# Performance work log

Measured on AMD Instinct MI355X. Metric: run time of the kernel, lower is better.

## Reference

```python
import jax, jax.numpy as jnp
import numpy as np

DIM = 192
HEADS = 4
EPS = 1e-12  # F.normalize default eps


def setup_inputs() -> dict:
    key = jax.random.key(0)
    ks = jax.random.split(key, 5)
    b, c, h, w = 8, DIM, 128, 128
    x = jax.random.normal(ks[0], (b, c, h, w), dtype=jnp.float32)
    w_qkv = jax.random.normal(ks[1], (3 * DIM, DIM, 1, 1), dtype=jnp.float32) * (1.0 / np.sqrt(DIM))
    w_dw = jax.random.normal(ks[2], (3 * DIM, 1, 3, 3), dtype=jnp.float32) * (1.0 / 3.0)
    w_proj = jax.random.normal(ks[3], (DIM, DIM, 1, 1), dtype=jnp.float32) * (1.0 / np.sqrt(DIM))
    temperature = jnp.ones((HEADS, 1, 1), dtype=jnp.float32)
    return {"x": x, "w_qkv": w_qkv, "w_dw": w_dw, "w_proj": w_proj, "temperature": temperature}


def _conv1x1(x, w):
    # x: [b,c,h,w], w: [o,c,1,1] -> [b,o,h,w]
    return jnp.einsum('bchw,oc->bohw', x, w[:, :, 0, 0])


def _dwconv3x3(x, w):
    # depthwise 3x3, padding=1; x: [b,C,h,w], w: [C,1,3,3]
    C = x.shape[1]
    return jax.lax.conv_general_dilated(
        x, w, window_strides=(1, 1), padding=((1, 1), (1, 1)),
        dimension_numbers=('NCHW', 'OIHW', 'NCHW'), feature_group_count=C)


def _l2norm(x):
    n = jnp.linalg.norm(x, axis=-1, keepdims=True)
    return x / jnp.maximum(n, EPS)


def reference(x, w_qkv, w_dw, w_proj, temperature):
    b, c, h, w = x.shape
    head = HEADS
    ch = c // head  # channels per head
    qkv = _dwconv3x3(_conv1x1(x, w_qkv), w_dw)  # [b, 3c, h, w]
    q, k, v = jnp.split(qkv, 3, axis=1)  # each [b, c, h, w]

    def to_heads(t):
        # b (head ch) h w -> b head h (ch w)
        t = t.reshape(b, head, ch, h, w)
        return t.transpose(0, 1, 3, 2, 4).reshape(b, head, h, ch * w)

    q1 = _l2norm(to_heads(q))
    k1 = _l2norm(to_heads(k))
    v1 = to_heads(v)
    # attn over height dim: [b, head, h, h]
    attn = jax.nn.softmax(jnp.einsum('bhif,bhjf->bhij', q1, k1) * temperature[None], axis=-1)
    out = jnp.einsum('bhij,bhjf->bhif', attn, v1)  # [b, head, h, ch*w]
    # b head h (ch w) -> b (head ch) h w
    out = out.reshape(b, head, h, ch, w).transpose(0, 1, 3, 2, 4).reshape(b, c, h, w)
    return _conv1x1(out, w_proj)
```

## Files before the change

### kernel.cpp

```cpp
#include <hip/hip_runtime.h>
#include <hip/hip_bf16.h>

#define BB 8
#define CC 192
#define C3 576
#define NH 4
#define CH 48
#define HH 128
#define WW 128
#define HW 16384
#define FF 6144

typedef short s16x8 __attribute__((ext_vector_type(8)));
typedef float f32x4 __attribute__((ext_vector_type(4)));

constexpr size_t SPM = 32ull * 128 * 128;

constexpr size_t OFF_XT  = 0;
constexpr size_t SZ_XT   = (size_t)BB * HW * CC * 2;
constexpr size_t OFF_WQ  = OFF_XT + SZ_XT;
constexpr size_t SZ_WQ   = (size_t)C3 * CC * 2;
constexpr size_t OFF_WP  = OFF_WQ + SZ_WQ;
constexpr size_t SZ_WP   = (size_t)CC * CC * 2;
constexpr size_t OFF_RAW = OFF_WP + SZ_WP;
constexpr size_t SZ_RAW  = (size_t)BB * C3 * HW * 2;
constexpr size_t OFF_DW  = OFF_RAW + SZ_RAW;
constexpr size_t OFF_SP  = OFF_DW + SZ_RAW;
constexpr size_t OFF_ATB = OFF_SP + 8 * SPM * 4;
constexpr size_t OFF_RQ  = OFF_ATB + 32ull * 128 * 128 * 2;
constexpr size_t OFF_RK  = OFF_RQ + 32 * 128 * 4;
constexpr size_t OFF_PS  = OFF_SP;

__device__ __forceinline__ short bf16bits(float v) {
  __hip_bfloat16 t = __float2bfloat16(v);
  return *reinterpret_cast<short*>(&t);
}
__device__ __forceinline__ float b2f(short u) {
  union { unsigned int i; float f; } x;
  x.i = ((unsigned int)(unsigned short)u) << 16;
  return x.f;
}

__device__ __forceinline__ void gload16(const void* g, void* l) {
  __builtin_amdgcn_global_load_lds((const __attribute__((address_space(1))) unsigned int*)g,
                                   (__attribute__((address_space(3))) unsigned int*)l, 16, 0, 0);
}

__device__ __forceinline__ void vmdrain() { asm volatile("s_waitcnt vmcnt(0)" ::: "memory"); }

__global__ __launch_bounds__(256) void k_cvt_t(const float* __restrict__ in,
                                               __hip_bfloat16* __restrict__ outT) {
  const int p0 = blockIdx.x * 64;
  const int c0 = blockIdx.y * 32;
  const int b = blockIdx.z;
  __shared__ float t[32][65];
  const float* ib = in + (size_t)b * CC * HW;
  const int tid = threadIdx.x;
  {
    const int c = tid >> 3, pl = (tid & 7) * 8;
    const float* s = ib + (size_t)(c0 + c) * HW + p0 + pl;
#pragma unroll
    for (int j = 0; j < 8; ++j) t[c][pl + j] = s[j];
  }
  __syncthreads();
  {
    const int pl = tid >> 2, cl = (tid & 3) * 8;
    __hip_bfloat16* d = outT + (size_t)b * HW * CC + (size_t)(p0 + pl) * CC + c0 + cl;
#pragma unroll
    for (int j = 0; j < 8; ++j) d[j] = __float2bfloat16(t[cl + j][pl]);
  }
}

__global__ __launch_bounds__(256) void k_cvt_w2(const float* __restrict__ in1, int n1,
                                                const float* __restrict__ in2, int n2,
                                                __hip_bfloat16* __restrict__ out) {
  const int i = blockIdx.x * 256 + threadIdx.x;
  if (i < n1) out[i] = __float2bfloat16(in1[i]);
  else if (i < n1 + n2) out[i] = __float2bfloat16(in2[i - n1]);
}

__global__ __launch_bounds__(256) void k_gemm(const __hip_bfloat16* __restrict__ xT,
                                              const __hip_bfloat16* __restrict__ Wb,
                                              __hip_bfloat16* __restrict__ out) {
  const int pBase = blockIdx.x * 128;
  const int mBase = blockIdx.y * 96;
  const int b = blockIdx.z;
  __shared__ char smem[28672];
  const int tid = threadIdx.x;
  const int wave = tid >> 6, lane = tid & 63;
  const int wm = wave >> 1, wn = wave & 1;
  const __hip_bfloat16* xb = xT + (size_t)b * HW * CC;
  f32x4 acc[3][4] = {};

  auto stage = [&](int k0, int buf) {
    char* Alc = smem + buf * 6144;
    char* Blc = smem + 12288 + buf * 8192;
    {
      const int ci = tid;
      const int row = ci & 15, kg = (ci >> 4) & 3, mf = ci >> 6;
      gload16(Wb + (size_t)(mBase + mf * 16 + row) * CC + k0 + kg * 8,
              Alc + wave * 1024);
    }
    if (tid < 128) {
      const int ci = 256 + tid;
      const int row = ci & 15, kg = (ci >> 4) & 3, mf = ci >> 6;
      gload16(Wb + (size_t)(mBase + mf * 16 + row) * CC + k0 + kg * 8,
              Alc + 4096 + wave * 1024);
    }
#pragma unroll
    for (int is = 0; is < 2; ++is) {
      const int ci = is * 256 + tid;
      const int col = ci & 15, kg = (ci >> 4) & 3, nf = ci >> 6;
      gload16(xb + (size_t)(pBase + nf * 16 + col) * CC + k0 + kg * 8,
              Blc + is * 4096 + wave * 1024);
    }
  };

  stage(0, 0);
  vmdrain();
  __syncthreads();
  for (int kc = 0; kc < 6; ++kc) {
    const int cur = kc & 1;
    if (kc < 5) stage((kc + 1) * 32, cur ^ 1);
    char* Alc = smem + cur * 6144;
    char* Blc = smem + 12288 + cur * 8192;
    s16x8 a[3], bf[4];
#pragma unroll
    for (int i = 0; i < 3; ++i) a[i] = *(const s16x8*)(Alc + ((wm * 3 + i) << 10) + (lane << 4));
#pragma unroll
    for (int j = 0; j < 4; ++j) bf[j] = *(const s16x8*)(Blc + ((wn * 4 + j) << 10) + (lane << 4));
#pragma unroll
    for (int i = 0; i < 3; ++i)
#pragma unroll
      for (int j = 0; j < 4; ++j)
        acc[i][j] = __builtin_amdgcn_mfma_f32_16x16x32_bf16(a[i], bf[j], acc[i][j], 0, 0, 0);
    vmdrain();
    __syncthreads();
  }
  short* E = (short*)smem;
  const int r0 = (lane >> 4) * 4, cl = lane & 15;
#pragma unroll
  for (int i = 0; i < 3; ++i) {
    const int lr = wm * 48 + i * 16 + r0;
#pragma unroll
    for (int j = 0; j < 4; ++j) {
      const int col = (wn * 4 + j) * 16 + cl;
#pragma unroll
      for (int r = 0; r < 4; ++r) E[(lr + r) * 136 + col] = bf16bits(acc[i][j][r]);
    }
  }
  __syncthreads();
  __hip_bfloat16* ob = out + (size_t)b * C3 * HW + pBase;
#pragma unroll
  for (int it = 0; it < 6; ++it) {
    const int vi = it * 256 + tid;
    const int row = vi >> 4, c8 = (vi & 15) * 8;
    const s16x8 v = *(const s16x8*)(E + row * 136 + c8);
    *(s16x8*)(ob + (size_t)(mBase + row) * HW + c8) = v;
  }
}

__global__ __launch_bounds__(256) void k_dwconv(const __hip_bfloat16* __restrict__ in,
                                                const float* __restrict__ wdw,
                                                __hip_bfloat16* __restrict__ out,
                                                __hip_bfloat16* __restrict__ vt,
                                                float* __restrict__ psum) {
  const int h0 = blockIdx.x * 32;
  const int c = blockIdx.y;
  const int b = blockIdx.z;
  __shared__ __hip_bfloat16 IN[34][152];
  __shared__ char TR[8192];
  const int tid = threadIdx.x;
  const __hip_bfloat16* src = in + ((size_t)b * C3 + c) * HW;
  if (tid < 68) {
    const int r = tid >> 1, col = (tid & 1) ? 136 : 0;
    *(s16x8*)(&IN[r][col]) = (s16x8){};
  }
#pragma unroll
  for (int it = 0; it < 3; ++it) {
    const int vi = it * 256 + tid;
    if (vi < 544) {
      const int r = vi >> 4, w8 = vi & 15;
      const int hg = h0 - 1 + r;
      s16x8 v = {};
      if (hg >= 0 && hg < HH) v = *(const s16x8*)(src + (size_t)hg * WW + w8 * 8);
      *(s16x8*)(&IN[r][8 + w8 * 8]) = v;
    }
  }
  const float* wp = wdw + c * 9;
  float wgt[9];
#pragma unroll
  for (int q = 0; q < 9; ++q) wgt[q] = wp[q];
  __syncthreads();

  const int hl = tid >> 3, w0 = (tid & 7) * 16;
  float res[16] = {};
#pragma unroll
  for (int dh = 0; dh < 3; ++dh) {
    const __hip_bfloat16* rp = &IN[hl + dh][0];
    const s16x8 v0 = *(const s16x8*)(rp + w0);
    const s16x8 v1 = *(const s16x8*)(rp + w0 + 8);
    const s16x8 v2 = *(const s16x8*)(rp + w0 + 16);
    const s16x8 v3 = *(const s16x8*)(rp + w0 + 24);
    float rv[18];
    rv[0] = b2f(v0[7]);
#pragma unroll
    for (int e = 0; e < 8; ++e) rv[1 + e] = b2f(v1[e]);
#pragma unroll
    for (int e = 0; e < 8; ++e) rv[9 + e] = b2f(v2[e]);
    rv[17] = b2f(v3[0]);
    const float wa = wgt[dh * 3], wb = wgt[dh * 3 + 1], wc = wgt[dh * 3 + 2];
#pragma unroll
    for (int ww = 0; ww < 16; ++ww)
      res[ww] += rv[ww] * wa + rv[ww + 1] * wb + rv[ww + 2] * wc;
  }
  if (c < 2 * CC) {
    short pk[16];
#pragma unroll
    for (int ww = 0; ww < 16; ++ww) pk[ww] = bf16bits(res[ww]);
    __hip_bfloat16* dst = out + ((size_t)b * C3 + c) * HW + (size_t)(h0 + hl) * WW + w0;
    *(s16x8*)dst = *(const s16x8*)pk;
    *(s16x8*)(dst + 8) = *(const s16x8*)(pk + 8);
    float ss = 0.f;
#pragma unroll
    for (int ww = 0; ww < 16; ++ww) ss += res[ww] * res[ww];
#pragma unroll
    for (int off = 4; off > 0; off >>= 1) ss += __shfl_down(ss, off);
    if ((tid & 7) == 0) psum[((size_t)b * HH + h0 + hl) * 384 + c] = ss;
  } else {
    const int rel = c - 2 * CC;
    const int hd = rel / CH, ch = rel - hd * CH;
#pragma unroll
    for (int ww = 0; ww < 16; ++ww) {
      const int w = w0 + ww;
      const int blk = ((w << 2) + (hl >> 3)) ^ ((w >> 3) & 3);
      *(short*)(TR + (blk << 4) + ((hl & 7) << 1)) = bf16bits(res[ww]);
    }
    __syncthreads();
    const int w = tid >> 1, hf = tid & 1;
    short ot[16];
#pragma unroll
    for (int j = 0; j < 2; ++j) {
      const int hh = hf * 16 + j * 8;
      const int blk = ((w << 2) + (hh >> 3)) ^ ((w >> 3) & 3);
      *(s16x8*)(ot + j * 8) = *(const s16x8*)(TR + (blk << 4));
    }
    __hip_bfloat16* vd = vt + ((size_t)(b * NH + hd) * FF + (size_t)ch * WW + w) * HH + h0 + hf * 16;
    *(s16x8*)vd = *(const s16x8*)ot;
    *(s16x8*)(vd + 8) = *(const s16x8*)(ot + 8);
  }
}

__global__ __launch_bounds__(64) void k_norms2(const float* __restrict__ psum,
                                               float* __restrict__ rq, float* __restrict__ rk) {
  const int i = blockIdx.x;
  const int hd = blockIdx.y;
  const int b = blockIdx.z & 7;
  const int which = blockIdx.z >> 3;
  const int lane = threadIdx.x;
  float s = 0.f;
  if (lane < 48) s = psum[((size_t)b * HH + i) * 384 + which * CC + hd * CH + lane];
#pragma unroll
  for (int off = 32; off > 0; off >>= 1) s += __shfl_down(s, off);
  if (lane == 0) {
    const float n = sqrtf(s);
    float* dst = which ? rk : rq;
    dst[(b * NH + hd) * HH + i] = 1.f / fmaxf(n, 1e-12f);
  }
}

__global__ __launch_bounds__(256) void k_qkm(const __hip_bfloat16* __restrict__ dw,
                                             float* __restrict__ sp) {
  const int ks = blockIdx.x;
  const int bh = blockIdx.y;
  const int b = bh >> 2, hd = bh & 3;
  const __hip_bfloat16* qb = dw + ((size_t)b * C3 + hd * CH) * HW;
  const __hip_bfloat16* kb = dw + ((size_t)b * C3 + CC + hd * CH) * HW;
  __shared__ __hip_bfloat16 Al[2][4096];
  __shared__ __hip_bfloat16 Bl[2][4096];
  const int tid = threadIdx.x, wave = tid >> 6, lane = tid & 63;
  const int wm = wave >> 1, wn = wave & 1;
  f32x4 acc[4][4] = {};

  auto stage = [&](int chunk, int buf) {
    const int ch = ks * 6 + (chunk >> 2);
    const int w0 = (chunk & 3) * 32;
    char* Alc = (char*)Al[buf];
    char* Blc = (char*)Bl[buf];
#pragma unroll
    for (int is = 0; is < 2; ++is) {
      const int ci = is * 256 + tid;
      const int row = ci & 15, kg = (ci >> 4) & 3, mf = ci >> 6;
      gload16(qb + (size_t)ch * HW + (mf * 16 + row) * WW + w0 + kg * 8,
              Alc + is * 4096 + wave * 1024);
    }
#pragma unroll
    for (int is = 0; is < 2; ++is) {
      const int ci = is * 256 + tid;
      const int col = ci & 15, kg = (ci >> 4) & 3, nf = ci >> 6;
      gload16(kb + (size_t)ch * HW + (nf * 16 + col) * WW + w0 + kg * 8,
              Blc + is * 4096 + wave * 1024);
    }
  };

  stage(0, 0);
  vmdrain();
  __syncthreads();
  for (int chunk = 0; chunk < 24; ++chunk) {
    const int cur = chunk & 1;
    if (chunk < 23) stage(chunk + 1, cur ^ 1);
    char* Alc = (char*)Al[cur];
    char* Blc = (char*)Bl[cur];
    s16x8 a[4], bf[4];
#pragma unroll
    for (int i = 0; i < 4; ++i) a[i] = *(const s16x8*)(Alc + ((wm * 4 + i) << 10) + (lane << 4));
#pragma unroll
    for (int j = 0; j < 4; ++j) bf[j] = *(const s16x8*)(Blc + ((wn * 4 + j) << 10) + (lane << 4));
#pragma unroll
    for (int i = 0; i < 4; ++i)
#pragma unroll
      for (int j = 0; j < 4; ++j)
        acc[i][j] = __builtin_amdgcn_mfma_f32_16x16x32_bf16(a[i], bf[j], acc[i][j], 0, 0, 0);
    vmdrain();
    __syncthreads();
  }
  float* o = sp + (size_t)ks * SPM + (size_t)bh * HH * HH;
  const int r0 = (lane >> 4) * 4, cl = lane & 15;
#pragma unroll
  for (int i = 0; i < 4; ++i)
#pragma unroll
    for (int j = 0; j < 4; ++j) {
      const int ii = wm * 64 + i * 16 + r0;
      const int jj = wn * 64 + j * 16 + cl;
#pragma unroll
      for (int r = 0; r < 4; ++r) o[(ii + r) * HH + jj] = acc[i][j][r];
    }
}

__global__ __launch_bounds__(256) void k_softmax(const float* __restrict__ sp,
                                                 const float* __restrict__ rq,
                                                 const float* __restrict__ rk,
                                                 const float* __restrict__ temp,
                                                 __hip_bfloat16* __restrict__ atb) {
  const int wave = threadIdx.x >> 6, lane = threadIdx.x & 63;
  const int i = blockIdx.x * 4 + wave;
  const int bh = blockIdx.y;
  const int hd = bh & 3;
  const size_t rowoff = ((size_t)bh * HH + i) * HH;
  float s0 = 0.f, s1 = 0.f;
#pragma unroll
  for (int ks = 0; ks < 8; ++ks) {
    s0 += sp[ks * SPM + rowoff + lane];
    s1 += sp[ks * SPM + rowoff + lane + 64];
  }
  const float scale = rq[bh * HH + i] * temp[hd];
  s0 *= scale * rk[bh * HH + lane];
  s1 *= scale * rk[bh * HH + lane + 64];
  float m = fmaxf(s0, s1);
#pragma unroll
  for (int off = 32; off > 0; off >>= 1) m = fmaxf(m, __shfl_xor(m, off));
  const float e0 = expf(s0 - m), e1 = expf(s1 - m);
  float ssum = e0 + e1;
#pragma unroll
  for (int off = 32; off > 0; off >>= 1) ssum += __shfl_xor(ssum, off);
  const float inv = 1.f / ssum;
  atb[rowoff + lane] = __float2bfloat16(e0 * inv);
  atb[rowoff + lane + 64] = __float2bfloat16(e1 * inv);
}

__global__ __launch_bounds__(256) void k_pvm(const __hip_bfloat16* __restrict__ atb,
                                             const __hip_bfloat16* __restrict__ vt,
                                             __hip_bfloat16* __restrict__ pvout) {
  const int fs = blockIdx.x;
  const int bh = blockIdx.y;
  const __hip_bfloat16* ab = atb + (size_t)bh * HH * HH;
  const __hip_bfloat16* vb = vt + ((size_t)bh * FF + fs * 128) * HH;
  __shared__ __hip_bfloat16 Al[2][4096];
  __shared__ __hip_bfloat16 Bl[2][4096];
  const int tid = threadIdx.x, wave = tid >> 6, lane = tid & 63;
  const int wm = wave >> 1, wn = wave & 1;
  f32x4 acc[4][4] = {};

  auto stage = [&](int kc, int buf) {
    const int kj0 = kc * 32;
    char* Alc = (char*)Al[buf];
    char* Blc = (char*)Bl[buf];
#pragma unroll
    for (int is = 0; is < 2; ++is) {
      const int ci = is * 256 + tid;
      const int row = ci & 15, kg = (ci >> 4) & 3, mf = ci >> 6;
      gload16(ab + (size_t)(mf * 16 + row) * HH + kj0 + kg * 8,
              Alc + is * 4096 + wave * 1024);
    }
#pragma unroll
    for (int is = 0; is < 2; ++is) {
      const int ci = is * 256 + tid;
      const int col = ci & 15, kg = (ci >> 4) & 3, nf = ci >> 6;
      gload16(vb + (size_t)(nf * 16 + col) * HH + kj0 + kg * 8,
              Blc + is * 4096 + wave * 1024);
    }
  };

  stage(0, 0);
  vmdrain();
  __syncthreads();
  for (int kc = 0; kc < 4; ++kc) {
    const int cur = kc & 1;
    if (kc < 3) stage(kc + 1, cur ^ 1);
    char* Alc = (char*)Al[cur];
    char* Blc = (char*)Bl[cur];
    s16x8 a[4], bf[4];
#pragma unroll
    for (int i = 0; i < 4; ++i) a[i] = *(const s16x8*)(Alc + ((wm * 4 + i) << 10) + (lane << 4));
#pragma unroll
    for (int j = 0; j < 4; ++j) bf[j] = *(const s16x8*)(Blc + ((wn * 4 + j) << 10) + (lane << 4));
#pragma unroll
    for (int i = 0; i < 4; ++i)
#pragma unroll
      for (int j = 0; j < 4; ++j)
        acc[i][j] = __builtin_amdgcn_mfma_f32_16x16x32_bf16(a[i], bf[j], acc[i][j], 0, 0, 0);
    vmdrain();
    __syncthreads();
  }
  __hip_bfloat16* ob = pvout + (size_t)bh * HH * FF;
  const int r0 = (lane >> 4) * 4, cl = lane & 15;
#pragma unroll
  for (int i = 0; i < 4; ++i)
#pragma unroll
    for (int j = 0; j < 4; ++j) {
      const int ii = wm * 64 + i * 16 + r0;
      const int f = fs * 128 + (wn * 4 + j) * 16 + cl;
#pragma unroll
      for (int r = 0; r < 4; ++r) ob[(size_t)(ii + r) * FF + f] = __float2bfloat16(acc[i][j][r]);
    }
}

__global__ __launch_bounds__(256) void k_proj(const __hip_bfloat16* __restrict__ pv,
                                              const __hip_bfloat16* __restrict__ Wp,
                                              float* __restrict__ out) {
  const int i = blockIdx.x;
  const int b = blockIdx.y;
  __shared__ __hip_bfloat16 Al[6144];
  __shared__ __hip_bfloat16 Braw[12288];
  __shared__ __hip_bfloat16 Bfrag[4096];
  char* Alc = (char*)Al;
  char* Brc = (char*)Braw;
  char* Bfc = (char*)Bfrag;
  const int tid = threadIdx.x, wave = tid >> 6, lane = tid & 63;
  const int wm = wave >> 1, wn = wave & 1;
  f32x4 acc[6][4] = {};
  for (int hf = 0; hf < 2; ++hf) {
    if (hf) __syncthreads();
#pragma unroll
    for (int it = 0; it < 6; ++it) {
      const int vi = it * 256 + tid;
      const int r = vi >> 4, w8 = vi & 15;
      const int hi = (r >= 48) ? 1 : 0;
      const int hd = hf * 2 + hi, ch = r - hi * 48;
      const s16x8 v = *(const s16x8*)(pv + ((size_t)(b * NH + hd) * HH + i) * FF + ch * 128 + w8 * 8);
      *(s16x8*)(Brc + r * 256 + ((w8 ^ (r & 15)) << 4)) = v;
    }
    __syncthreads();
    for (int kc = 0; kc < 3; ++kc) {
      const int c0 = hf * 96 + kc * 32;
#pragma unroll
      for (int is = 0; is < 3; ++is) {
        const int ci = is * 256 + tid;
        const int row = ci & 15, kg = (ci >> 4) & 3, mf = ci >> 6;
        gload16(Wp + (size_t)(mf * 16 + row) * CC + c0 + kg * 8,
                Alc + is * 4096 + wave * 1024);
      }
#pragma unroll
      for (int it = 0; it < 2; ++it) {
        const int vi = it * 256 + tid;
        const int col = vi & 15, kg = (vi >> 4) & 3, nf = vi >> 6;
        const int w = nf * 16 + col;
        short tmp[8];
#pragma unroll
        for (int e = 0; e < 8; ++e) {
          const int r = (kc * 4 + kg) * 8 + e;
          tmp[e] = *(const short*)(Brc + r * 256 + (((w >> 3) ^ (r & 15)) << 4) + (w & 7) * 2);
        }
        *(s16x8*)(Bfc + ((nf * 64 + kg * 16 + col) << 4)) = *(const s16x8*)tmp;
      }
      vmdrain();
      __syncthreads();
      s16x8 a[6], bf[4];
#pragma unroll
      for (int mi = 0; mi < 6; ++mi)
        a[mi] = *(const s16x8*)(Alc + ((wm * 6 + mi) << 10) + (lane << 4));
#pragma unroll
      for (int j = 0; j < 4; ++j)
        bf[j] = *(const s16x8*)(Bfc + (((wn * 4 + j) * 64 + lane) << 4));
#pragma unroll
      for (int mi = 0; mi < 6; ++mi)
#pragma unroll
        for (int j = 0; j < 4; ++j)
          acc[mi][j] = __builtin_amdgcn_mfma_f32_16x16x32_bf16(a[mi], bf[j], acc[mi][j], 0, 0, 0);
      __syncthreads();
    }
  }
  const int r0 = (lane >> 4) * 4, cl = lane & 15;
#pragma unroll
  for (int mi = 0; mi < 6; ++mi) {
    const int o = (wm * 6 + mi) * 16 + r0;
#pragma unroll
    for (int j = 0; j < 4; ++j) {
      const int w = (wn * 4 + j) * 16 + cl;
      float* dst = out + ((size_t)b * CC + o) * HW + i * 128 + w;
#pragma unroll
      for (int r = 0; r < 4; ++r) dst[(size_t)r * HW] = acc[mi][j][r];
    }
  }
}

extern "C" void kernel_launch(void* const* d_in, const int* in_sizes, int n_in,
                              void* d_out, int out_size, void* d_ws, size_t ws_size,
                              hipStream_t stream) {
  const float* x     = (const float*)d_in[0];
  const float* wqkv  = (const float*)d_in[1];
  const float* wdw   = (const float*)d_in[2];
  const float* wproj = (const float*)d_in[3];
  const float* temp  = (const float*)d_in[4];

  char* ws = (char*)d_ws;
  __hip_bfloat16* xTb    = (__hip_bfloat16*)(ws + OFF_XT);
  __hip_bfloat16* vt     = (__hip_bfloat16*)(ws + OFF_XT);
  __hip_bfloat16* Wq     = (__hip_bfloat16*)(ws + OFF_WQ);
  __hip_bfloat16* Wp     = (__hip_bfloat16*)(ws + OFF_WP);
  __hip_bfloat16* qkvraw = (__hip_bfloat16*)(ws + OFF_RAW);
  __hip_bfloat16* pvout  = (__hip_bfloat16*)(ws + OFF_RAW);
  __hip_bfloat16* qkvdw  = (__hip_bfloat16*)(ws + OFF_DW);
  float* sp    = (float*)(ws + OFF_SP);
  float* psum  = (float*)(ws + OFF_PS);
  __hip_bfloat16* atb = (__hip_bfloat16*)(ws + OFF_ATB);
  float* rq    = (float*)(ws + OFF_RQ);
  float* rk    = (float*)(ws + OFF_RK);

  k_cvt_w2<<<dim3((C3 * CC + CC * CC + 255) / 256), 256, 0, stream>>>(wqkv, C3 * CC, wproj, CC * CC, Wq);
  k_cvt_t<<<dim3(HW / 64, CC / 32, BB), 256, 0, stream>>>(x, xTb);
  k_gemm<<<dim3(HW / 128, C3 / 96, BB), 256, 0, stream>>>(xTb, Wq, qkvraw);
  k_dwconv<<<dim3(HH / 32, C3, BB), 256, 0, stream>>>(qkvraw, wdw, qkvdw, vt, psum);
  k_norms2<<<dim3(HH, NH, 2 * BB), 64, 0, stream>>>(psum, rq, rk);
  k_qkm<<<dim3(8, 32), 256, 0, stream>>>(qkvdw, sp);
  k_softmax<<<dim3(HH / 4, 32), 256, 0, stream>>>(sp, rq, rk, temp, atb);
  k_pvm<<<dim3(48, 32), 256, 0, stream>>>(atb, vt, pvout);
  k_proj<<<dim3(HH, BB), 256, 0, stream>>>(pvout, Wp, (float*)d_out);
}
```

Baseline: 271.7 us.

## Triple-buffer LDS staging with partial vmcnt waits in GEMM kernels

Switches the qkv GEMM, the QK^T kernel and the PV kernel from double-buffered to triple-buffered LDS staging. Loads now run two stages ahead, and the full vmcnt(0) drain plus __syncthreads is replaced by per-wave partial vmcnt waits and raw s_barrier calls. The aim is to keep global-to-LDS loads in flight while MFMAs run, hiding memory latency. In exchange the kernels use more shared memory, which may lower occupancy, and correctness depends on hand-counted vmcnt values per wave.

```diff
diff --git a/kernel.cpp b/kernel.cpp
--- a/kernel.cpp
+++ b/kernel.cpp
@@ -46,6 +46,7 @@
                                    (__attribute__((address_space(3))) unsigned int*)l, 16, 0, 0);
 }
 
+#define VMWAIT(N) asm volatile("s_waitcnt vmcnt(" #N ")" ::: "memory")
 __device__ __forceinline__ void vmdrain() { asm volatile("s_waitcnt vmcnt(0)" ::: "memory"); }
 
 __global__ __launch_bounds__(256) void k_cvt_t(const float* __restrict__ in,
@@ -85,7 +86,7 @@
   const int pBase = blockIdx.x * 128;
   const int mBase = blockIdx.y * 96;
   const int b = blockIdx.z;
-  __shared__ char smem[28672];
+  __shared__ char smem[43008];
   const int tid = threadIdx.x;
   const int wave = tid >> 6, lane = tid & 63;
   const int wm = wave >> 1, wn = wave & 1;
@@ -93,19 +94,17 @@
   f32x4 acc[3][4] = {};
 
   auto stage = [&](int k0, int buf) {
-    char* Alc = smem + buf * 6144;
-    char* Blc = smem + 12288 + buf * 8192;
+    char* Alc = smem + buf * 14336;
+    char* Blc = Alc + 6144;
     {
       const int ci = tid;
       const int row = ci & 15, kg = (ci >> 4) & 3, mf = ci >> 6;
-      gload16(Wb + (size_t)(mBase + mf * 16 + row) * CC + k0 + kg * 8,
-              Alc + wave * 1024);
+      gload16(Wb + (size_t)(mBase + mf * 16 + row) * CC + k0 + kg * 8, Alc + wave * 1024);
     }
     if (tid < 128) {
       const int ci = 256 + tid;
       const int row = ci & 15, kg = (ci >> 4) & 3, mf = ci >> 6;
-      gload16(Wb + (size_t)(mBase + mf * 16 + row) * CC + k0 + kg * 8,
-              Alc + 4096 + wave * 1024);
+      gload16(Wb + (size_t)(mBase + mf * 16 + row) * CC + k0 + kg * 8, Alc + 4096 + wave * 1024);
     }
 #pragma unroll
     for (int is = 0; is < 2; ++is) {
@@ -117,13 +116,17 @@
   };
 
   stage(0, 0);
-  vmdrain();
-  __syncthreads();
+  stage(32, 1);
+#pragma unroll
   for (int kc = 0; kc < 6; ++kc) {
-    const int cur = kc & 1;
-    if (kc < 5) stage((kc + 1) * 32, cur ^ 1);
-    char* Alc = smem + cur * 6144;
-    char* Blc = smem + 12288 + cur * 8192;
+    const int cur = kc % 3;
+    if (kc < 4) stage((kc + 2) * 32, (kc + 2) % 3);
+    if (kc < 4) { if (wave < 2) VMWAIT(8); else VMWAIT(6); }
+    else if (kc == 4) { if (wave < 2) VMWAIT(4); else VMWAIT(3); }
+    else VMWAIT(0);
+    __builtin_amdgcn_s_barrier();
+    char* Alc = smem + cur * 14336;
+    char* Blc = Alc + 6144;
     s16x8 a[3], bf[4];
 #pragma unroll
     for (int i = 0; i < 3; ++i) a[i] = *(const s16x8*)(Alc + ((wm * 3 + i) << 10) + (lane << 4));
@@ -134,8 +137,7 @@
 #pragma unroll
       for (int j = 0; j < 4; ++j)
         acc[i][j] = __builtin_amdgcn_mfma_f32_16x16x32_bf16(a[i], bf[j], acc[i][j], 0, 0, 0);
-    vmdrain();
-    __syncthreads();
+    __builtin_amdgcn_s_barrier();
   }
   short* E = (short*)smem;
   const int r0 = (lane >> 4) * 4, cl = lane & 15;
@@ -276,8 +278,7 @@
   const int b = bh >> 2, hd = bh & 3;
   const __hip_bfloat16* qb = dw + ((size_t)b * C3 + hd * CH) * HW;
   const __hip_bfloat16* kb = dw + ((size_t)b * C3 + CC + hd * CH) * HW;
-  __shared__ __hip_bfloat16 Al[2][4096];
-  __shared__ __hip_bfloat16 Bl[2][4096];
+  __shared__ char smem[49152];
   const int tid = threadIdx.x, wave = tid >> 6, lane = tid & 63;
   const int wm = wave >> 1, wn = wave & 1;
   f32x4 acc[4][4] = {};
@@ -285,8 +286,8 @@
   auto stage = [&](int chunk, int buf) {
     const int ch = ks * 6 + (chunk >> 2);
     const int w0 = (chunk & 3) * 32;
-    char* Alc = (char*)Al[buf];
-    char* Blc = (char*)Bl[buf];
+    char* Alc = smem + buf * 16384;
+    char* Blc = Alc + 8192;
 #pragma unroll
     for (int is = 0; is < 2; ++is) {
       const int ci = is * 256 + tid;
@@ -304,13 +305,15 @@
   };
 
   stage(0, 0);
-  vmdrain();
-  __syncthreads();
+  stage(1, 1);
   for (int chunk = 0; chunk < 24; ++chunk) {
-    const int cur = chunk & 1;
-    if (chunk < 23) stage(chunk + 1, cur ^ 1);
-    char* Alc = (char*)Al[cur];
-    char* Blc = (char*)Bl[cur];
+    if (chunk < 22) stage(chunk + 2, (chunk + 2) % 3);
+    if (chunk < 22) VMWAIT(8);
+    else if (chunk == 22) VMWAIT(4);
+    else VMWAIT(0);
+    __builtin_amdgcn_s_barrier();
+    char* Alc = smem + (chunk % 3) * 16384;
+    char* Blc = Alc + 8192;
     s16x8 a[4], bf[4];
 #pragma unroll
     for (int i = 0; i < 4; ++i) a[i] = *(const s16x8*)(Alc + ((wm * 4 + i) << 10) + (lane << 4));
@@ -321,8 +324,7 @@
 #pragma unroll
       for (int j = 0; j < 4; ++j)
         acc[i][j] = __builtin_amdgcn_mfma_f32_16x16x32_bf16(a[i], bf[j], acc[i][j], 0, 0, 0);
-    vmdrain();
-    __syncthreads();
+    __builtin_amdgcn_s_barrier();
   }
   float* o = sp + (size_t)ks * SPM + (size_t)bh * HH * HH;
   const int r0 = (lane >> 4) * 4, cl = lane & 15;
@@ -375,16 +377,15 @@
   const int bh = blockIdx.y;
   const __hip_bfloat16* ab = atb + (size_t)bh * HH * HH;
   const __hip_bfloat16* vb = vt + ((size_t)bh * FF + fs * 128) * HH;
-  __shared__ __hip_bfloat16 Al[2][4096];
-  __shared__ __hip_bfloat16 Bl[2][4096];
+  __shared__ char smem[49152];
   const int tid = threadIdx.x, wave = tid >> 6, lane = tid & 63;
   const int wm = wave >> 1, wn = wave & 1;
   f32x4 acc[4][4] = {};
 
   auto stage = [&](int kc, int buf) {
     const int kj0 = kc * 32;
-    char* Alc = (char*)Al[buf];
-    char* Blc = (char*)Bl[buf];
+    char* Alc = smem + buf * 16384;
+    char* Blc = Alc + 8192;
 #pragma unroll
     for (int is = 0; is < 2; ++is) {
       const int ci = is * 256 + tid;
@@ -402,13 +403,16 @@
   };
 
   stage(0, 0);
-  vmdrain();
-  __syncthreads();
+  stage(1, 1);
+#pragma unroll
   for (int kc = 0; kc < 4; ++kc) {
-    const int cur = kc & 1;
-    if (kc < 3) stage(kc + 1, cur ^ 1);
-    char* Alc = (char*)Al[cur];
-    char* Blc = (char*)Bl[cur];
+    if (kc < 2) stage(kc + 2, (kc + 2) % 3);
+    if (kc < 2) VMWAIT(8);
+    else if (kc == 2) VMWAIT(4);
+    else VMWAIT(0);
+    __builtin_amdgcn_s_barrier();
+    char* Alc = smem + (kc % 3) * 16384;
+    char* Blc = Alc + 8192;
     s16x8 a[4], bf[4];
 #pragma unroll
     for (int i = 0; i < 4; ++i) a[i] = *(const s16x8*)(Alc + ((wm * 4 + i) << 10) + (lane << 4));
@@ -419,8 +423,7 @@
 #pragma unroll
       for (int j = 0; j < 4; ++j)
         acc[i][j] = __builtin_amdgcn_mfma_f32_16x16x32_bf16(a[i], bf[j], acc[i][j], 0, 0, 0);
-    vmdrain();
-    __syncthreads();
+    __builtin_amdgcn_s_barrier();
   }
   __hip_bfloat16* ob = pvout + (size_t)bh * HH * FF;
   const int r0 = (lane >> 4) * 4, cl = lane & 15;
```

New measurement: 261.7 us. 3.7% less time.
